# Kernel optimization log

Hardware: AMD Instinct MI355X
Metric: run time of the kernel (lower is better)

Reference implementation:

```python
import jax, jax.numpy as jnp
import numpy as np

B, S, H = 2, 2048, 1024
E, I, K = 8, 4096, 2


def setup_inputs() -> dict:
    key = jax.random.key(0)
    ks = jax.random.split(key, 5)
    scale_h = 1.0 / np.sqrt(H)
    scale_i = 1.0 / np.sqrt(I)
    x = jax.random.normal(ks[0], (B, S, H), dtype=jnp.float32)
    gate_w = jax.random.normal(ks[1], (E, H), dtype=jnp.float32) * scale_h   # router Linear weight [out=E, in=H]
    wg = jax.random.normal(ks[2], (E, I, H), dtype=jnp.float32) * scale_h    # gate_proj weights, stacked over experts
    wu = jax.random.normal(ks[3], (E, I, H), dtype=jnp.float32) * scale_h    # up_proj weights
    wd = jax.random.normal(ks[4], (E, H, I), dtype=jnp.float32) * scale_i    # down_proj weights
    return {"x": x, "gate_w": gate_w, "wg": wg, "wu": wu, "wd": wd}


def _moe_forward(x, gate_w, wg, wu, wd):
    b, s, h = x.shape
    x_flat = x.reshape(-1, h)                       # [T, H]
    logits = x_flat @ gate_w.T                      # [T, E]
    top_v, top_i = jax.lax.top_k(logits, K)         # [T, K]
    probs = jax.nn.softmax(top_v.astype(jnp.float32), axis=-1).astype(logits.dtype)  # [T, K]
    # per-token combine weight for each expert: sum_k probs[:,k] * 1[top_i[:,k]==e]
    one_hot = jax.nn.one_hot(top_i, E, dtype=probs.dtype)   # [T, K, E]
    combine = jnp.einsum('tk,tke->et', probs, one_hot)       # [E, T]
    # loop over experts via scan: acc += w_e * SwiGLU_e(x)
    def body(acc, ws):
        wge, wue, wde, we = ws
        hidden = jax.nn.silu(x_flat @ wge.T) * (x_flat @ wue.T)  # [T, I]
        return acc + we[:, None] * (hidden @ wde.T), None
    out, _ = jax.lax.scan(body, jnp.zeros_like(x_flat), (wg, wu, wd, combine))
    return out.reshape(b, s, h)


def reference(x, gate_w, wg, wu, wd):
    return _moe_forward(x, gate_w, wg, wu, wd)
```

## Files before the change

kernel.cpp:

```cpp
#include <hip/hip_runtime.h>
#include <math.h>

#define T_TOK 4096
#define H_DIM 1024
#define E_NUM 8
#define I_DIM 4096

typedef __attribute__((ext_vector_type(4))) float f32x4;
typedef __attribute__((ext_vector_type(8))) short bf16x8;

__device__ inline unsigned short f2bf(float f) {
  unsigned int u = __float_as_uint(f);
  u += 0x7fffu + ((u >> 16) & 1u);
  return (unsigned short)(u >> 16);
}

__device__ inline void cvt_store4(unsigned short* dst, const float* src) {
  f32x4 v = *reinterpret_cast<const f32x4*>(src);
  ushort4 o;
  o.x = f2bf(v[0]); o.y = f2bf(v[1]); o.z = f2bf(v[2]); o.w = f2bf(v[3]);
  *reinterpret_cast<ushort4*>(dst) = o;
}

__device__ inline void gll16(const void* g, void* l) {
  __builtin_amdgcn_global_load_lds(
      (const __attribute__((address_space(1))) void*)g,
      (__attribute__((address_space(3))) void*)l, 16, 0, 0);
}

__global__ __launch_bounds__(64) void k_router(const float* __restrict__ x,
                                               const float* __restrict__ gw,
                                               int2* __restrict__ tokE,
                                               float2* __restrict__ tokP,
                                               int* __restrict__ counts) {
  const int t = blockIdx.x;
  const int l = threadIdx.x;
  const float* xr = x + (size_t)t * H_DIM;
  float acc[E_NUM];
#pragma unroll
  for (int e = 0; e < E_NUM; e++) acc[e] = 0.f;
  for (int h = l; h < H_DIM; h += 64) {
    float xv = xr[h];
#pragma unroll
    for (int e = 0; e < E_NUM; e++) acc[e] += xv * gw[e * H_DIM + h];
  }
#pragma unroll
  for (int e = 0; e < E_NUM; e++) {
#pragma unroll
    for (int off = 32; off > 0; off >>= 1) acc[e] += __shfl_xor(acc[e], off);
  }
  if (l == 0) {
    float v0 = -1e30f, v1 = -1e30f;
    int e0 = 0, e1 = 0;
#pragma unroll
    for (int e = 0; e < E_NUM; e++) {
      float v = acc[e];
      if (v > v0) { v1 = v0; e1 = e0; v0 = v; e0 = e; }
      else if (v > v1) { v1 = v; e1 = e; }
    }
    float ex = expf(v1 - v0);
    float p0 = 1.f / (1.f + ex);
    float p1 = ex * p0;
    tokE[t] = make_int2(e0, e1);
    tokP[t] = make_float2(p0, p1);
    atomicAdd(&counts[e0], 1);
    atomicAdd(&counts[e1], 1);
  }
}

__global__ void k_offsets(const int* __restrict__ counts, int* __restrict__ offsets) {
  if (threadIdx.x == 0 && blockIdx.x == 0) {
    int s = 0;
    for (int e = 0; e < E_NUM; e++) { offsets[e] = s; s += counts[e]; }
    offsets[E_NUM] = s;
  }
}

__global__ __launch_bounds__(256) void k_scatter(const int2* __restrict__ tokE,
                                                 const float2* __restrict__ tokP,
                                                 const int* __restrict__ offsets,
                                                 int* __restrict__ cursor,
                                                 int* __restrict__ slot_tok,
                                                 float* __restrict__ slot_w) {
  int t = blockIdx.x * 256 + threadIdx.x;
  if (t >= T_TOK) return;
  int2 e = tokE[t];
  float2 p = tokP[t];
  int pos0 = atomicAdd(&cursor[e.x], 1);
  slot_tok[offsets[e.x] + pos0] = t;
  slot_w[offsets[e.x] + pos0] = p.x;
  int pos1 = atomicAdd(&cursor[e.y], 1);
  slot_tok[offsets[e.y] + pos1] = t;
  slot_w[offsets[e.y] + pos1] = p.y;
}

__global__ __launch_bounds__(256) void k_cvt(const float* __restrict__ src,
                                             unsigned short* __restrict__ dst,
                                             int n4) {
  int i = blockIdx.x * 256 + threadIdx.x;
  const int stride = gridDim.x * 256;
  for (; i < n4; i += stride) {
    f32x4 v = reinterpret_cast<const f32x4*>(src)[i];
    ushort4 o;
    o.x = f2bf(v[0]); o.y = f2bf(v[1]); o.z = f2bf(v[2]); o.w = f2bf(v[3]);
    reinterpret_cast<ushort4*>(dst)[i] = o;
  }
}

__global__ __launch_bounds__(256, 2) void k_gateup2(
    const unsigned short* __restrict__ xb, const unsigned short* __restrict__ wgb,
    const unsigned short* __restrict__ wub, const int* __restrict__ counts,
    const int* __restrict__ offsets, const int* __restrict__ slot_tok,
    unsigned short* __restrict__ hidden) {
  const int e = blockIdx.z;
  const int cnt = counts[e];
  const int m0 = blockIdx.y * 128;
  if (m0 >= cnt) return;
  const int n0 = blockIdx.x * 128;
  const int base = offsets[e];

  __shared__ unsigned short As[128 * 64];
  __shared__ unsigned short Bg[128 * 64];
  __shared__ unsigned short Bu[128 * 64];

  const int tid = threadIdx.x;
  const int wave = tid >> 6;
  const int lane = tid & 63;
  const int wm = (wave >> 1) * 64;
  const int wn = (wave & 1) * 64;
  const int lr = lane & 15;
  const int lk = lane >> 4;

  const int sr = lane >> 3;
  const int sc = lane & 7;
  const int swz = ((sc ^ sr) << 3);

  const size_t wbase = (size_t)e * I_DIM * H_DIM;
  const unsigned short* srcA[4];
  const unsigned short* srcBg[4];
  const unsigned short* srcBu[4];
  unsigned short* dstA[4];
  unsigned short* dstBg[4];
  unsigned short* dstBu[4];
#pragma unroll
  for (int i = 0; i < 4; i++) {
    int row = wave * 32 + i * 8 + sr;
    int gr = m0 + row; if (gr > cnt - 1) gr = cnt - 1;
    srcA[i]  = xb + (size_t)slot_tok[base + gr] * H_DIM + swz;
    srcBg[i] = wgb + wbase + (size_t)(n0 + row) * H_DIM + swz;
    srcBu[i] = wub + wbase + (size_t)(n0 + row) * H_DIM + swz;
    dstA[i]  = &As[(wave * 32 + i * 8) * 64];
    dstBg[i] = &Bg[(wave * 32 + i * 8) * 64];
    dstBu[i] = &Bu[(wave * 32 + i * 8) * 64];
  }

  f32x4 accg[4][4], accu[4][4];
#pragma unroll
  for (int i = 0; i < 4; i++)
#pragma unroll
    for (int j = 0; j < 4; j++) {
      accg[i][j] = (f32x4){0.f, 0.f, 0.f, 0.f};
      accu[i][j] = (f32x4){0.f, 0.f, 0.f, 0.f};
    }

  const int xorr = ((lr & 7) << 3);

  for (int k0 = 0; k0 < H_DIM; k0 += 64) {
#pragma unroll
    for (int i = 0; i < 4; i++) {
      gll16(srcA[i] + k0, dstA[i]);
      gll16(srcBg[i] + k0, dstBg[i]);
      gll16(srcBu[i] + k0, dstBu[i]);
    }
    __syncthreads();
#pragma unroll
    for (int kh = 0; kh < 2; kh++) {
      const int koff = (((kh * 4 + lk) << 3) ^ xorr);
      bf16x8 af[4];
#pragma unroll
      for (int mf = 0; mf < 4; mf++)
        af[mf] = *reinterpret_cast<const bf16x8*>(&As[(wm + mf * 16 + lr) * 64 + koff]);
#pragma unroll
      for (int nf = 0; nf < 4; nf++) {
        const int roff = (wn + nf * 16 + lr) * 64 + koff;
        bf16x8 bg = *reinterpret_cast<const bf16x8*>(&Bg[roff]);
        bf16x8 bu = *reinterpret_cast<const bf16x8*>(&Bu[roff]);
#pragma unroll
        for (int mf = 0; mf < 4; mf++) {
          accg[mf][nf] = __builtin_amdgcn_mfma_f32_16x16x32_bf16(af[mf], bg, accg[mf][nf], 0, 0, 0);
          accu[mf][nf] = __builtin_amdgcn_mfma_f32_16x16x32_bf16(af[mf], bu, accu[mf][nf], 0, 0, 0);
        }
      }
    }
    __syncthreads();
  }

#pragma unroll
  for (int mf = 0; mf < 4; mf++) {
#pragma unroll
    for (int j = 0; j < 4; j++) {
      int row = wm + mf * 16 + lk * 4 + j;
      if (m0 + row < cnt) {
        size_t hbase = (size_t)(base + m0 + row) * I_DIM;
#pragma unroll
        for (int nf = 0; nf < 4; nf++) {
          int col = n0 + wn + nf * 16 + lr;
          float g = accg[mf][nf][j];
          float u = accu[mf][nf][j];
          float h = g / (1.f + expf(-g)) * u;
          hidden[hbase + col] = f2bf(h);
        }
      }
    }
  }
}

__global__ __launch_bounds__(256, 2) void k_down2(
    const unsigned short* __restrict__ hidden, const unsigned short* __restrict__ wdb,
    const int* __restrict__ counts, const int* __restrict__ offsets,
    const int* __restrict__ slot_tok, const float* __restrict__ slot_w,
    float* __restrict__ out) {
  const int e = blockIdx.z;
  const int cnt = counts[e];
  const int m0 = blockIdx.y * 128;
  if (m0 >= cnt) return;
  const int n0 = blockIdx.x * 128;
  const int base = offsets[e];

  __shared__ unsigned short As[128 * 64];
  __shared__ unsigned short Bs[128 * 64];

  const int tid = threadIdx.x;
  const int wave = tid >> 6;
  const int lane = tid & 63;
  const int wm = (wave >> 1) * 64;
  const int wn = (wave & 1) * 64;
  const int lr = lane & 15;
  const int lk = lane >> 4;

  const int sr = lane >> 3;
  const int sc = lane & 7;
  const int swz = ((sc ^ sr) << 3);

  const unsigned short* srcA[4];
  const unsigned short* srcB[4];
  unsigned short* dstA[4];
  unsigned short* dstB[4];
#pragma unroll
  for (int i = 0; i < 4; i++) {
    int row = wave * 32 + i * 8 + sr;
    int gr = m0 + row; if (gr > cnt - 1) gr = cnt - 1;
    srcA[i] = hidden + (size_t)(base + gr) * I_DIM + swz;
    srcB[i] = wdb + (size_t)e * H_DIM * I_DIM + (size_t)(n0 + row) * I_DIM + swz;
    dstA[i] = &As[(wave * 32 + i * 8) * 64];
    dstB[i] = &Bs[(wave * 32 + i * 8) * 64];
  }

  f32x4 acc[4][4];
#pragma unroll
  for (int i = 0; i < 4; i++)
#pragma unroll
    for (int j = 0; j < 4; j++) acc[i][j] = (f32x4){0.f, 0.f, 0.f, 0.f};

  const int xorr = ((lr & 7) << 3);

  for (int k0 = 0; k0 < I_DIM; k0 += 64) {
#pragma unroll
    for (int i = 0; i < 4; i++) {
      gll16(srcA[i] + k0, dstA[i]);
      gll16(srcB[i] + k0, dstB[i]);
    }
    __syncthreads();
#pragma unroll
    for (int kh = 0; kh < 2; kh++) {
      const int koff = (((kh * 4 + lk) << 3) ^ xorr);
      bf16x8 af[4];
#pragma unroll
      for (int mf = 0; mf < 4; mf++)
        af[mf] = *reinterpret_cast<const bf16x8*>(&As[(wm + mf * 16 + lr) * 64 + koff]);
#pragma unroll
      for (int nf = 0; nf < 4; nf++) {
        bf16x8 bf = *reinterpret_cast<const bf16x8*>(&Bs[(wn + nf * 16 + lr) * 64 + koff]);
#pragma unroll
        for (int mf = 0; mf < 4; mf++)
          acc[mf][nf] = __builtin_amdgcn_mfma_f32_16x16x32_bf16(af[mf], bf, acc[mf][nf], 0, 0, 0);
      }
    }
    __syncthreads();
  }

#pragma unroll
  for (int mf = 0; mf < 4; mf++) {
#pragma unroll
    for (int j = 0; j < 4; j++) {
      int row = wm + mf * 16 + lk * 4 + j;
      if (m0 + row < cnt) {
        int slot = base + m0 + row;
        int t = slot_tok[slot];
        float w = slot_w[slot];
#pragma unroll
        for (int nf = 0; nf < 4; nf++) {
          int col = n0 + wn + nf * 16 + lr;
          atomicAdd(&out[(size_t)t * H_DIM + col], w * acc[mf][nf][j]);
        }
      }
    }
  }
}

__global__ __launch_bounds__(256) void k_gateup_v1(
    const float* __restrict__ x, const float* __restrict__ wg,
    const float* __restrict__ wu, const int* __restrict__ counts,
    const int* __restrict__ offsets, const int* __restrict__ slot_tok,
    unsigned short* __restrict__ hidden) {
  const int e = blockIdx.z;
  const int cnt = counts[e];
  const int m0 = blockIdx.y * 128;
  if (m0 >= cnt) return;
  const int n0 = blockIdx.x * 128;
  const int base = offsets[e];

  __shared__ unsigned short As[128 * 40];
  __shared__ unsigned short Bgs[128 * 40];
  __shared__ unsigned short Bus[128 * 40];

  const int tid = threadIdx.x;
  const int wave = tid >> 6;
  const int lane = tid & 63;
  const int wm = (wave >> 1) * 64;
  const int wn = (wave & 1) * 64;
  const int lr = lane & 15;
  const int lk = lane >> 4;
  const int r_sub = tid >> 3;
  const int kq = (tid & 7) * 4;

  const float* wge = wg + (size_t)e * I_DIM * H_DIM;
  const float* wue = wu + (size_t)e * I_DIM * H_DIM;

  const float* aptr[4];
  const float* bgptr[4];
  const float* buptr[4];
#pragma unroll
  for (int p = 0; p < 4; p++) {
    int row = p * 32 + r_sub;
    int gr = m0 + row;
    if (gr > cnt - 1) gr = cnt - 1;
    aptr[p] = x + (size_t)slot_tok[base + gr] * H_DIM + kq;
    bgptr[p] = wge + (size_t)(n0 + row) * H_DIM + kq;
    buptr[p] = wue + (size_t)(n0 + row) * H_DIM + kq;
  }

  f32x4 accg[4][4], accu[4][4];
#pragma unroll
  for (int i = 0; i < 4; i++)
#pragma unroll
    for (int j = 0; j < 4; j++) {
      accg[i][j] = (f32x4){0.f, 0.f, 0.f, 0.f};
      accu[i][j] = (f32x4){0.f, 0.f, 0.f, 0.f};
    }

  for (int k0 = 0; k0 < H_DIM; k0 += 32) {
#pragma unroll
    for (int p = 0; p < 4; p++) {
      int row = p * 32 + r_sub;
      cvt_store4(&As[row * 40 + kq], aptr[p] + k0);
      cvt_store4(&Bgs[row * 40 + kq], bgptr[p] + k0);
      cvt_store4(&Bus[row * 40 + kq], buptr[p] + k0);
    }
    __syncthreads();
    bf16x8 af[4];
#pragma unroll
    for (int mf = 0; mf < 4; mf++)
      af[mf] = *reinterpret_cast<const bf16x8*>(&As[(wm + mf * 16 + lr) * 40 + lk * 8]);
#pragma unroll
    for (int nf = 0; nf < 4; nf++) {
      bf16x8 bg = *reinterpret_cast<const bf16x8*>(&Bgs[(wn + nf * 16 + lr) * 40 + lk * 8]);
      bf16x8 bu = *reinterpret_cast<const bf16x8*>(&Bus[(wn + nf * 16 + lr) * 40 + lk * 8]);
#pragma unroll
      for (int mf = 0; mf < 4; mf++) {
        accg[mf][nf] = __builtin_amdgcn_mfma_f32_16x16x32_bf16(af[mf], bg, accg[mf][nf], 0, 0, 0);
        accu[mf][nf] = __builtin_amdgcn_mfma_f32_16x16x32_bf16(af[mf], bu, accu[mf][nf], 0, 0, 0);
      }
    }
    __syncthreads();
  }

#pragma unroll
  for (int mf = 0; mf < 4; mf++) {
#pragma unroll
    for (int j = 0; j < 4; j++) {
      int row = wm + mf * 16 + lk * 4 + j;
      if (m0 + row < cnt) {
        size_t hbase = (size_t)(base + m0 + row) * I_DIM;
#pragma unroll
        for (int nf = 0; nf < 4; nf++) {
          int col = n0 + wn + nf * 16 + lr;
          float g = accg[mf][nf][j];
          float u = accu[mf][nf][j];
          float h = g / (1.f + expf(-g)) * u;
          hidden[hbase + col] = f2bf(h);
        }
      }
    }
  }
}

__global__ __launch_bounds__(256) void k_down_v1(
    const unsigned short* __restrict__ hidden, const float* __restrict__ wd,
    const int* __restrict__ counts, const int* __restrict__ offsets,
    const int* __restrict__ slot_tok, const float* __restrict__ slot_w,
    float* __restrict__ out) {
  const int e = blockIdx.z;
  const int cnt = counts[e];
  const int m0 = blockIdx.y * 128;
  if (m0 >= cnt) return;
  const int n0 = blockIdx.x * 128;
  const int base = offsets[e];

  __shared__ unsigned short As[128 * 40];
  __shared__ unsigned short Bs[128 * 40];

  const int tid = threadIdx.x;
  const int wave = tid >> 6;
  const int lane = tid & 63;
  const int wm = (wave >> 1) * 64;
  const int wn = (wave & 1) * 64;
  const int lr = lane & 15;
  const int lk = lane >> 4;
  const int r_sub = tid >> 3;
  const int kq = (tid & 7) * 4;

  const unsigned short* ap[4];
  const float* bp[4];
#pragma unroll
  for (int p = 0; p < 4; p++) {
    int row = p * 32 + r_sub;
    int gr = m0 + row;
    if (gr > cnt - 1) gr = cnt - 1;
    ap[p] = hidden + (size_t)(base + gr) * I_DIM + kq;
    bp[p] = wd + (size_t)e * H_DIM * I_DIM + (size_t)(n0 + row) * I_DIM + kq;
  }

  f32x4 acc[4][4];
#pragma unroll
  for (int i = 0; i < 4; i++)
#pragma unroll
    for (int j = 0; j < 4; j++) acc[i][j] = (f32x4){0.f, 0.f, 0.f, 0.f};

  for (int k0 = 0; k0 < I_DIM; k0 += 32) {
#pragma unroll
    for (int p = 0; p < 4; p++) {
      int row = p * 32 + r_sub;
      *reinterpret_cast<ushort4*>(&As[row * 40 + kq]) =
          *reinterpret_cast<const ushort4*>(ap[p] + k0);
      cvt_store4(&Bs[row * 40 + kq], bp[p] + k0);
    }
    __syncthreads();
    bf16x8 af[4];
#pragma unroll
    for (int mf = 0; mf < 4; mf++)
      af[mf] = *reinterpret_cast<const bf16x8*>(&As[(wm + mf * 16 + lr) * 40 + lk * 8]);
#pragma unroll
    for (int nf = 0; nf < 4; nf++) {
      bf16x8 bf = *reinterpret_cast<const bf16x8*>(&Bs[(wn + nf * 16 + lr) * 40 + lk * 8]);
#pragma unroll
      for (int mf = 0; mf < 4; mf++)
        acc[mf][nf] = __builtin_amdgcn_mfma_f32_16x16x32_bf16(af[mf], bf, acc[mf][nf], 0, 0, 0);
    }
    __syncthreads();
  }

#pragma unroll
  for (int mf = 0; mf < 4; mf++) {
#pragma unroll
    for (int j = 0; j < 4; j++) {
      int row = wm + mf * 16 + lk * 4 + j;
      if (m0 + row < cnt) {
        int slot = base + m0 + row;
        int t = slot_tok[slot];
        float w = slot_w[slot];
#pragma unroll
        for (int nf = 0; nf < 4; nf++) {
          int col = n0 + wn + nf * 16 + lr;
          atomicAdd(&out[(size_t)t * H_DIM + col], w * acc[mf][nf][j]);
        }
      }
    }
  }
}

extern "C" void kernel_launch(void* const* d_in, const int* in_sizes, int n_in,
                              void* d_out, int out_size, void* d_ws, size_t ws_size,
                              hipStream_t stream) {
  const float* x = (const float*)d_in[0];
  const float* gate_w = (const float*)d_in[1];
  const float* wg = (const float*)d_in[2];
  const float* wu = (const float*)d_in[3];
  const float* wd = (const float*)d_in[4];
  float* out = (float*)d_out;

  char* ws = (char*)d_ws;
  int* counts = (int*)(ws + 0);
  int* cursor = (int*)(ws + 64);
  int* offsets = (int*)(ws + 128);
  int2* tokE = (int2*)(ws + 256);
  float2* tokP = (float2*)(ws + 256 + 32768);
  int* slot_tok = (int*)(ws + 256 + 65536);
  float* slot_w = (float*)(ws + 256 + 98304);

  hipMemsetAsync(d_ws, 0, 256, stream);
  hipMemsetAsync(d_out, 0, (size_t)T_TOK * H_DIM * sizeof(float), stream);

  k_router<<<T_TOK, 64, 0, stream>>>(x, gate_w, tokE, tokP, counts);
  k_offsets<<<1, 64, 0, stream>>>(counts, offsets);
  k_scatter<<<T_TOK / 256, 256, 0, stream>>>(tokE, tokP, offsets, cursor, slot_tok, slot_w);

  const size_t OFF_XB  = 262144;
  const size_t OFF_HID = OFF_XB + 8388608;
  const size_t OFF_WG  = OFF_HID + 67108864;
  const size_t OFF_WU  = OFF_WG + 67108864;
  const size_t NEED    = OFF_WU + 67108864;

  if (ws_size >= NEED) {
    unsigned short* xb  = (unsigned short*)(ws + OFF_XB);
    unsigned short* hid = (unsigned short*)(ws + OFF_HID);
    unsigned short* wgb = (unsigned short*)(ws + OFF_WG);
    unsigned short* wub = (unsigned short*)(ws + OFF_WU);
    unsigned short* wdb = wgb;

    k_cvt<<<2048, 256, 0, stream>>>(x, xb, T_TOK * H_DIM / 4);
    k_cvt<<<2048, 256, 0, stream>>>(wg, wgb, E_NUM * I_DIM * H_DIM / 4);
    k_cvt<<<2048, 256, 0, stream>>>(wu, wub, E_NUM * I_DIM * H_DIM / 4);
    k_gateup2<<<dim3(I_DIM / 128, 32, E_NUM), 256, 0, stream>>>(
        xb, wgb, wub, counts, offsets, slot_tok, hid);
    k_cvt<<<2048, 256, 0, stream>>>(wd, wdb, E_NUM * H_DIM * I_DIM / 4);
    k_down2<<<dim3(H_DIM / 128, 32, E_NUM), 256, 0, stream>>>(
        hid, wdb, counts, offsets, slot_tok, slot_w, out);
  } else {
    unsigned short* hid = (unsigned short*)(ws + 131328);
    k_gateup_v1<<<dim3(I_DIM / 128, 32, E_NUM), 256, 0, stream>>>(
        x, wg, wu, counts, offsets, slot_tok, hid);
    k_down_v1<<<dim3(H_DIM / 128, 32, E_NUM), 256, 0, stream>>>(
        hid, wd, counts, offsets, slot_tok, slot_w, out);
  }
}
```

Measured before the change: 563.5 us.

## Rewrite MoE GEMMs as 8-wave double-buffered 256x128 tiles with phased prefetch

```diff
diff --git a/kernel.cpp b/kernel.cpp
--- a/kernel.cpp
+++ b/kernel.cpp
@@ -107,190 +107,279 @@
   }
 }
 
-__global__ __launch_bounds__(256, 2) void k_gateup2(
+
+__global__ __launch_bounds__(512, 2) void k_gateup8(
     const unsigned short* __restrict__ xb, const unsigned short* __restrict__ wgb,
     const unsigned short* __restrict__ wub, const int* __restrict__ counts,
     const int* __restrict__ offsets, const int* __restrict__ slot_tok,
     unsigned short* __restrict__ hidden) {
   const int e = blockIdx.z;
   const int cnt = counts[e];
-  const int m0 = blockIdx.y * 128;
+  const int m0 = blockIdx.y * 256;
   if (m0 >= cnt) return;
   const int n0 = blockIdx.x * 128;
   const int base = offsets[e];
 
-  __shared__ unsigned short As[128 * 64];
-  __shared__ unsigned short Bg[128 * 64];
-  __shared__ unsigned short Bu[128 * 64];
+  __shared__ unsigned short As[2][256 * 64];
+  __shared__ unsigned short Bgs[2][128 * 64];
+  __shared__ unsigned short Bus[2][128 * 64];
 
   const int tid = threadIdx.x;
   const int wave = tid >> 6;
   const int lane = tid & 63;
-  const int wm = (wave >> 1) * 64;
-  const int wn = (wave & 1) * 64;
+  const int wm = (wave >> 2) * 128;
+  const int wn = (wave & 3) * 32;
   const int lr = lane & 15;
   const int lk = lane >> 4;
-
-  const int sr = lane >> 3;
-  const int sc = lane & 7;
-  const int swz = ((sc ^ sr) << 3);
-
-  const size_t wbase = (size_t)e * I_DIM * H_DIM;
-  const unsigned short* srcA[4];
-  const unsigned short* srcBg[4];
-  const unsigned short* srcBu[4];
-  unsigned short* dstA[4];
-  unsigned short* dstBg[4];
-  unsigned short* dstBu[4];
+  const int xr = lr & 7;
+
+  const int srow = lane >> 3;
+  const int schk = lane & 7;
+  const int swz = ((schk ^ srow) << 3);
+  const int ldsw = wave * 8 * 64;
+
+  const size_t wboff = (size_t)e * (size_t)I_DIM * H_DIM;
+  const unsigned short* pA[4];
+  const unsigned short* pBg[2];
+  const unsigned short* pBu[2];
 #pragma unroll
   for (int i = 0; i < 4; i++) {
-    int row = wave * 32 + i * 8 + sr;
-    int gr = m0 + row; if (gr > cnt - 1) gr = cnt - 1;
-    srcA[i]  = xb + (size_t)slot_tok[base + gr] * H_DIM + swz;
-    srcBg[i] = wgb + wbase + (size_t)(n0 + row) * H_DIM + swz;
-    srcBu[i] = wub + wbase + (size_t)(n0 + row) * H_DIM + swz;
-    dstA[i]  = &As[(wave * 32 + i * 8) * 64];
-    dstBg[i] = &Bg[(wave * 32 + i * 8) * 64];
-    dstBu[i] = &Bu[(wave * 32 + i * 8) * 64];
-  }
-
-  f32x4 accg[4][4], accu[4][4];
-#pragma unroll
-  for (int i = 0; i < 4; i++)
-#pragma unroll
-    for (int j = 0; j < 4; j++) {
+    int r = i * 64 + wave * 8 + srow;
+    int gr = m0 + r; if (gr > cnt - 1) gr = cnt - 1;
+    pA[i] = xb + (size_t)slot_tok[base + gr] * H_DIM + swz;
+  }
+#pragma unroll
+  for (int i = 0; i < 2; i++) {
+    int r = i * 64 + wave * 8 + srow;
+    pBg[i] = wgb + wboff + (size_t)(n0 + r) * H_DIM + swz;
+    pBu[i] = wub + wboff + (size_t)(n0 + r) * H_DIM + swz;
+  }
+
+  f32x4 accg[8][2], accu[8][2];
+#pragma unroll
+  for (int i = 0; i < 8; i++)
+#pragma unroll
+    for (int j = 0; j < 2; j++) {
       accg[i][j] = (f32x4){0.f, 0.f, 0.f, 0.f};
       accu[i][j] = (f32x4){0.f, 0.f, 0.f, 0.f};
     }
 
-  const int xorr = ((lr & 7) << 3);
-
-  for (int k0 = 0; k0 < H_DIM; k0 += 64) {
-#pragma unroll
-    for (int i = 0; i < 4; i++) {
-      gll16(srcA[i] + k0, dstA[i]);
-      gll16(srcBg[i] + k0, dstBg[i]);
-      gll16(srcBu[i] + k0, dstBu[i]);
-    }
-    __syncthreads();
-#pragma unroll
-    for (int kh = 0; kh < 2; kh++) {
-      const int koff = (((kh * 4 + lk) << 3) ^ xorr);
-      bf16x8 af[4];
-#pragma unroll
-      for (int mf = 0; mf < 4; mf++)
-        af[mf] = *reinterpret_cast<const bf16x8*>(&As[(wm + mf * 16 + lr) * 64 + koff]);
-#pragma unroll
-      for (int nf = 0; nf < 4; nf++) {
-        const int roff = (wn + nf * 16 + lr) * 64 + koff;
-        bf16x8 bg = *reinterpret_cast<const bf16x8*>(&Bg[roff]);
-        bf16x8 bu = *reinterpret_cast<const bf16x8*>(&Bu[roff]);
-#pragma unroll
-        for (int mf = 0; mf < 4; mf++) {
-          accg[mf][nf] = __builtin_amdgcn_mfma_f32_16x16x32_bf16(af[mf], bg, accg[mf][nf], 0, 0, 0);
-          accu[mf][nf] = __builtin_amdgcn_mfma_f32_16x16x32_bf16(af[mf], bu, accu[mf][nf], 0, 0, 0);
-        }
-      }
-    }
-    __syncthreads();
-  }
-
-#pragma unroll
-  for (int mf = 0; mf < 4; mf++) {
+  const int ar = (wm + lr) * 64;
+  const int br = (wn + lr) * 64;
+  const int c0 = ((lk ^ xr) << 3);
+  const int c1 = (((4 + lk) ^ xr) << 3);
+
+  bf16x8 fg[2][2], fu[2][2];
+
+  gll16(pBg[0], &Bgs[0][0 * 4096 + ldsw]);
+  gll16(pBg[1], &Bgs[0][1 * 4096 + ldsw]);
+  gll16(pBu[0], &Bus[0][0 * 4096 + ldsw]);
+  gll16(pBu[1], &Bus[0][1 * 4096 + ldsw]);
+  gll16(pA[0], &As[0][0 * 4096 + ldsw]);
+  gll16(pA[2], &As[0][2 * 4096 + ldsw]);
+  gll16(pA[1], &As[0][1 * 4096 + ldsw]);
+  gll16(pA[3], &As[0][3 * 4096 + ldsw]);
+
+#define GU_PHASE(P, CUR, NXT, KNXT)                                            \
+  do {                                                                         \
+    if ((P) == 0) {                                                            \
+      gll16(pBg[0] + (KNXT), &Bgs[NXT][0 * 4096 + ldsw]);                      \
+      gll16(pBg[1] + (KNXT), &Bgs[NXT][1 * 4096 + ldsw]);                      \
+      asm volatile("s_waitcnt vmcnt(4)" ::: "memory");                         \
+    } else if ((P) == 1) {                                                     \
+      gll16(pBu[0] + (KNXT), &Bus[NXT][0 * 4096 + ldsw]);                      \
+      gll16(pBu[1] + (KNXT), &Bus[NXT][1 * 4096 + ldsw]);                      \
+    } else if ((P) == 2) {                                                     \
+      gll16(pA[0] + (KNXT), &As[NXT][0 * 4096 + ldsw]);                        \
+      gll16(pA[2] + (KNXT), &As[NXT][2 * 4096 + ldsw]);                        \
+      asm volatile("s_waitcnt vmcnt(6)" ::: "memory");                         \
+    } else {                                                                   \
+      gll16(pA[1] + (KNXT), &As[NXT][1 * 4096 + ldsw]);                        \
+      gll16(pA[3] + (KNXT), &As[NXT][3 * 4096 + ldsw]);                        \
+    }                                                                          \
+    __builtin_amdgcn_s_barrier();                                              \
+    if ((P) == 0) {                                                            \
+      _Pragma("unroll") for (int nf = 0; nf < 2; nf++) {                       \
+        fg[nf][0] = *(const bf16x8*)&Bgs[CUR][br + nf * 1024 + c0];            \
+        fg[nf][1] = *(const bf16x8*)&Bgs[CUR][br + nf * 1024 + c1];            \
+        fu[nf][0] = *(const bf16x8*)&Bus[CUR][br + nf * 1024 + c0];            \
+        fu[nf][1] = *(const bf16x8*)&Bus[CUR][br + nf * 1024 + c1];            \
+      }                                                                        \
+    }                                                                          \
+    bf16x8 a00 = *(const bf16x8*)&As[CUR][ar + (2 * (P)) * 1024 + c0];         \
+    bf16x8 a01 = *(const bf16x8*)&As[CUR][ar + (2 * (P)) * 1024 + c1];         \
+    bf16x8 a10 = *(const bf16x8*)&As[CUR][ar + (2 * (P) + 1) * 1024 + c0];     \
+    bf16x8 a11 = *(const bf16x8*)&As[CUR][ar + (2 * (P) + 1) * 1024 + c1];     \
+    __builtin_amdgcn_s_setprio(1);                                             \
+    _Pragma("unroll") for (int nf = 0; nf < 2; nf++) {                         \
+      accg[2*(P)][nf]   = __builtin_amdgcn_mfma_f32_16x16x32_bf16(a00, fg[nf][0], accg[2*(P)][nf], 0, 0, 0);     \
+      accg[2*(P)][nf]   = __builtin_amdgcn_mfma_f32_16x16x32_bf16(a01, fg[nf][1], accg[2*(P)][nf], 0, 0, 0);     \
+      accu[2*(P)][nf]   = __builtin_amdgcn_mfma_f32_16x16x32_bf16(a00, fu[nf][0], accu[2*(P)][nf], 0, 0, 0);     \
+      accu[2*(P)][nf]   = __builtin_amdgcn_mfma_f32_16x16x32_bf16(a01, fu[nf][1], accu[2*(P)][nf], 0, 0, 0);     \
+      accg[2*(P)+1][nf] = __builtin_amdgcn_mfma_f32_16x16x32_bf16(a10, fg[nf][0], accg[2*(P)+1][nf], 0, 0, 0);   \
+      accg[2*(P)+1][nf] = __builtin_amdgcn_mfma_f32_16x16x32_bf16(a11, fg[nf][1], accg[2*(P)+1][nf], 0, 0, 0);   \
+      accu[2*(P)+1][nf] = __builtin_amdgcn_mfma_f32_16x16x32_bf16(a10, fu[nf][0], accu[2*(P)+1][nf], 0, 0, 0);   \
+      accu[2*(P)+1][nf] = __builtin_amdgcn_mfma_f32_16x16x32_bf16(a11, fu[nf][1], accu[2*(P)+1][nf], 0, 0, 0);   \
+    }                                                                          \
+    __builtin_amdgcn_s_setprio(0);                                             \
+    __builtin_amdgcn_s_barrier();                                              \
+  } while (0)
+
+#define GU_STEP(CUR, NXT, KNXT) \
+  GU_PHASE(0, CUR, NXT, KNXT);  \
+  GU_PHASE(1, CUR, NXT, KNXT);  \
+  GU_PHASE(2, CUR, NXT, KNXT);  \
+  GU_PHASE(3, CUR, NXT, KNXT);
+
+  for (int t = 0; t < 16; t += 2) {
+    const int k1 = (t + 1) * 64;
+    const int k2 = (t + 2 < 16) ? (t + 2) * 64 : 0;
+    GU_STEP(0, 1, k1);
+    GU_STEP(1, 0, k2);
+  }
+#undef GU_PHASE
+#undef GU_STEP
+
+#pragma unroll
+  for (int mf = 0; mf < 8; mf++) {
 #pragma unroll
     for (int j = 0; j < 4; j++) {
       int row = wm + mf * 16 + lk * 4 + j;
       if (m0 + row < cnt) {
         size_t hbase = (size_t)(base + m0 + row) * I_DIM;
 #pragma unroll
-        for (int nf = 0; nf < 4; nf++) {
+        for (int nf = 0; nf < 2; nf++) {
           int col = n0 + wn + nf * 16 + lr;
           float g = accg[mf][nf][j];
           float u = accu[mf][nf][j];
-          float h = g / (1.f + expf(-g)) * u;
-          hidden[hbase + col] = f2bf(h);
+          hidden[hbase + col] = f2bf(g / (1.f + expf(-g)) * u);
         }
       }
     }
   }
 }
 
-__global__ __launch_bounds__(256, 2) void k_down2(
+__global__ __launch_bounds__(512, 2) void k_down8(
     const unsigned short* __restrict__ hidden, const unsigned short* __restrict__ wdb,
     const int* __restrict__ counts, const int* __restrict__ offsets,
     const int* __restrict__ slot_tok, const float* __restrict__ slot_w,
     float* __restrict__ out) {
   const int e = blockIdx.z;
   const int cnt = counts[e];
-  const int m0 = blockIdx.y * 128;
+  const int m0 = blockIdx.y * 256;
   if (m0 >= cnt) return;
   const int n0 = blockIdx.x * 128;
   const int base = offsets[e];
 
-  __shared__ unsigned short As[128 * 64];
-  __shared__ unsigned short Bs[128 * 64];
+  __shared__ unsigned short As[2][256 * 64];
+  __shared__ unsigned short Bs[2][128 * 64];
 
   const int tid = threadIdx.x;
   const int wave = tid >> 6;
   const int lane = tid & 63;
-  const int wm = (wave >> 1) * 64;
-  const int wn = (wave & 1) * 64;
+  const int wm = (wave >> 2) * 128;
+  const int wn = (wave & 3) * 32;
   const int lr = lane & 15;
   const int lk = lane >> 4;
-
-  const int sr = lane >> 3;
-  const int sc = lane & 7;
-  const int swz = ((sc ^ sr) << 3);
-
-  const unsigned short* srcA[4];
-  const unsigned short* srcB[4];
-  unsigned short* dstA[4];
-  unsigned short* dstB[4];
+  const int xr = lr & 7;
+
+  const int srow = lane >> 3;
+  const int schk = lane & 7;
+  const int swz = ((schk ^ srow) << 3);
+  const int ldsw = wave * 8 * 64;
+
+  const unsigned short* pA[4];
+  const unsigned short* pB[2];
 #pragma unroll
   for (int i = 0; i < 4; i++) {
-    int row = wave * 32 + i * 8 + sr;
-    int gr = m0 + row; if (gr > cnt - 1) gr = cnt - 1;
-    srcA[i] = hidden + (size_t)(base + gr) * I_DIM + swz;
-    srcB[i] = wdb + (size_t)e * H_DIM * I_DIM + (size_t)(n0 + row) * I_DIM + swz;
-    dstA[i] = &As[(wave * 32 + i * 8) * 64];
-    dstB[i] = &Bs[(wave * 32 + i * 8) * 64];
-  }
-
-  f32x4 acc[4][4];
-#pragma unroll
-  for (int i = 0; i < 4; i++)
-#pragma unroll
-    for (int j = 0; j < 4; j++) acc[i][j] = (f32x4){0.f, 0.f, 0.f, 0.f};
-
-  const int xorr = ((lr & 7) << 3);
-
-  for (int k0 = 0; k0 < I_DIM; k0 += 64) {
-#pragma unroll
-    for (int i = 0; i < 4; i++) {
-      gll16(srcA[i] + k0, dstA[i]);
-      gll16(srcB[i] + k0, dstB[i]);
-    }
-    __syncthreads();
-#pragma unroll
-    for (int kh = 0; kh < 2; kh++) {
-      const int koff = (((kh * 4 + lk) << 3) ^ xorr);
-      bf16x8 af[4];
-#pragma unroll
-      for (int mf = 0; mf < 4; mf++)
-        af[mf] = *reinterpret_cast<const bf16x8*>(&As[(wm + mf * 16 + lr) * 64 + koff]);
-#pragma unroll
-      for (int nf = 0; nf < 4; nf++) {
-        bf16x8 bf = *reinterpret_cast<const bf16x8*>(&Bs[(wn + nf * 16 + lr) * 64 + koff]);
-#pragma unroll
-        for (int mf = 0; mf < 4; mf++)
-          acc[mf][nf] = __builtin_amdgcn_mfma_f32_16x16x32_bf16(af[mf], bf, acc[mf][nf], 0, 0, 0);
-      }
-    }
-    __syncthreads();
-  }
-
-#pragma unroll
-  for (int mf = 0; mf < 4; mf++) {
+    int r = i * 64 + wave * 8 + srow;
+    int gr = m0 + r; if (gr > cnt - 1) gr = cnt - 1;
+    pA[i] = hidden + (size_t)(base + gr) * I_DIM + swz;
+  }
+#pragma unroll
+  for (int i = 0; i < 2; i++) {
+    int r = i * 64 + wave * 8 + srow;
+    pB[i] = wdb + (size_t)e * H_DIM * I_DIM + (size_t)(n0 + r) * I_DIM + swz;
+  }
+
+  f32x4 acc[8][2];
+#pragma unroll
+  for (int i = 0; i < 8; i++)
+#pragma unroll
+    for (int j = 0; j < 2; j++) acc[i][j] = (f32x4){0.f, 0.f, 0.f, 0.f};
+
+  const int ar = (wm + lr) * 64;
+  const int br = (wn + lr) * 64;
+  const int c0 = ((lk ^ xr) << 3);
+  const int c1 = (((4 + lk) ^ xr) << 3);
+
+  bf16x8 fb[2][2];
+
+  gll16(pB[0], &Bs[0][0 * 4096 + ldsw]);
+  gll16(pB[1], &Bs[0][1 * 4096 + ldsw]);
+  gll16(pA[0], &As[0][0 * 4096 + ldsw]);
+  gll16(pA[2], &As[0][2 * 4096 + ldsw]);
+  gll16(pA[1], &As[0][1 * 4096 + ldsw]);
+  gll16(pA[3], &As[0][3 * 4096 + ldsw]);
+
+#define DN_PHASE(P, CUR, NXT, KNXT)                                            \
+  do {                                                                         \
+    if ((P) == 0) {                                                            \
+      gll16(pB[0] + (KNXT), &Bs[NXT][0 * 4096 + ldsw]);                        \
+      gll16(pB[1] + (KNXT), &Bs[NXT][1 * 4096 + ldsw]);                        \
+      gll16(pA[0] + (KNXT), &As[NXT][0 * 4096 + ldsw]);                        \
+      asm volatile("s_waitcnt vmcnt(5)" ::: "memory");                         \
+    } else {                                                                   \
+      gll16(pA[2] + (KNXT), &As[NXT][2 * 4096 + ldsw]);                        \
+      gll16(pA[1] + (KNXT), &As[NXT][1 * 4096 + ldsw]);                        \
+      gll16(pA[3] + (KNXT), &As[NXT][3 * 4096 + ldsw]);                        \
+      asm volatile("s_waitcnt vmcnt(6)" ::: "memory");                         \
+    }                                                                          \
+    __builtin_amdgcn_s_barrier();                                              \
+    if ((P) == 0) {                                                            \
+      _Pragma("unroll") for (int nf = 0; nf < 2; nf++) {                       \
+        fb[nf][0] = *(const bf16x8*)&Bs[CUR][br + nf * 1024 + c0];             \
+        fb[nf][1] = *(const bf16x8*)&Bs[CUR][br + nf * 1024 + c1];             \
+      }                                                                        \
+    }                                                                          \
+    bf16x8 a0k0 = *(const bf16x8*)&As[CUR][ar + (4 * (P) + 0) * 1024 + c0];    \
+    bf16x8 a0k1 = *(const bf16x8*)&As[CUR][ar + (4 * (P) + 0) * 1024 + c1];    \
+    bf16x8 a1k0 = *(const bf16x8*)&As[CUR][ar + (4 * (P) + 1) * 1024 + c0];    \
+    bf16x8 a1k1 = *(const bf16x8*)&As[CUR][ar + (4 * (P) + 1) * 1024 + c1];    \
+    bf16x8 a2k0 = *(const bf16x8*)&As[CUR][ar + (4 * (P) + 2) * 1024 + c0];    \
+    bf16x8 a2k1 = *(const bf16x8*)&As[CUR][ar + (4 * (P) + 2) * 1024 + c1];    \
+    bf16x8 a3k0 = *(const bf16x8*)&As[CUR][ar + (4 * (P) + 3) * 1024 + c0];    \
+    bf16x8 a3k1 = *(const bf16x8*)&As[CUR][ar + (4 * (P) + 3) * 1024 + c1];    \
+    __builtin_amdgcn_s_setprio(1);                                             \
+    _Pragma("unroll") for (int nf = 0; nf < 2; nf++) {                         \
+      acc[4*(P)+0][nf] = __builtin_amdgcn_mfma_f32_16x16x32_bf16(a0k0, fb[nf][0], acc[4*(P)+0][nf], 0, 0, 0);  \
+      acc[4*(P)+0][nf] = __builtin_amdgcn_mfma_f32_16x16x32_bf16(a0k1, fb[nf][1], acc[4*(P)+0][nf], 0, 0, 0);  \
+      acc[4*(P)+1][nf] = __builtin_amdgcn_mfma_f32_16x16x32_bf16(a1k0, fb[nf][0], acc[4*(P)+1][nf], 0, 0, 0);  \
+      acc[4*(P)+1][nf] = __builtin_amdgcn_mfma_f32_16x16x32_bf16(a1k1, fb[nf][1], acc[4*(P)+1][nf], 0, 0, 0);  \
+      acc[4*(P)+2][nf] = __builtin_amdgcn_mfma_f32_16x16x32_bf16(a2k0, fb[nf][0], acc[4*(P)+2][nf], 0, 0, 0);  \
+      acc[4*(P)+2][nf] = __builtin_amdgcn_mfma_f32_16x16x32_bf16(a2k1, fb[nf][1], acc[4*(P)+2][nf], 0, 0, 0);  \
+      acc[4*(P)+3][nf] = __builtin_amdgcn_mfma_f32_16x16x32_bf16(a3k0, fb[nf][0], acc[4*(P)+3][nf], 0, 0, 0);  \
+      acc[4*(P)+3][nf] = __builtin_amdgcn_mfma_f32_16x16x32_bf16(a3k1, fb[nf][1], acc[4*(P)+3][nf], 0, 0, 0);  \
+    }                                                                          \
+    __builtin_amdgcn_s_setprio(0);                                             \
+    __builtin_amdgcn_s_barrier();                                              \
+  } while (0)
+
+#define DN_STEP(CUR, NXT, KNXT) \
+  DN_PHASE(0, CUR, NXT, KNXT);  \
+  DN_PHASE(1, CUR, NXT, KNXT);
+
+  for (int t = 0; t < 64; t += 2) {
+    const int k1 = (t + 1) * 64;
+    const int k2 = (t + 2 < 64) ? (t + 2) * 64 : 0;
+    DN_STEP(0, 1, k1);
+    DN_STEP(1, 0, k2);
+  }
+#undef DN_PHASE
+#undef DN_STEP
+
+#pragma unroll
+  for (int mf = 0; mf < 8; mf++) {
 #pragma unroll
     for (int j = 0; j < 4; j++) {
       int row = wm + mf * 16 + lk * 4 + j;
@@ -299,7 +388,7 @@
         int t = slot_tok[slot];
         float w = slot_w[slot];
 #pragma unroll
-        for (int nf = 0; nf < 4; nf++) {
+        for (int nf = 0; nf < 2; nf++) {
           int col = n0 + wn + nf * 16 + lr;
           atomicAdd(&out[(size_t)t * H_DIM + col], w * acc[mf][nf][j]);
         }
@@ -531,10 +620,10 @@
     k_cvt<<<2048, 256, 0, stream>>>(x, xb, T_TOK * H_DIM / 4);
     k_cvt<<<2048, 256, 0, stream>>>(wg, wgb, E_NUM * I_DIM * H_DIM / 4);
     k_cvt<<<2048, 256, 0, stream>>>(wu, wub, E_NUM * I_DIM * H_DIM / 4);
-    k_gateup2<<<dim3(I_DIM / 128, 32, E_NUM), 256, 0, stream>>>(
+    k_gateup8<<<dim3(I_DIM / 128, 16, E_NUM), 512, 0, stream>>>(
         xb, wgb, wub, counts, offsets, slot_tok, hid);
     k_cvt<<<2048, 256, 0, stream>>>(wd, wdb, E_NUM * H_DIM * I_DIM / 4);
-    k_down2<<<dim3(H_DIM / 128, 32, E_NUM), 256, 0, stream>>>(
+    k_down8<<<dim3(H_DIM / 128, 16, E_NUM), 512, 0, stream>>>(
         hid, wdb, counts, offsets, slot_tok, slot_w, out);
   } else {
     unsigned short* hid = (unsigned short*)(ws + 131328);
```

Result: slower. 695.3 us (+23.4%).

## Double-buffer LDS tiles with async prefetch in gate-up and down GEMMs

Applied to the files above, without the earlier changes.

```diff
diff --git a/kernel.cpp b/kernel.cpp
--- a/kernel.cpp
+++ b/kernel.cpp
@@ -107,7 +107,8 @@
   }
 }
 
-__global__ __launch_bounds__(256, 2) void k_gateup2(
+
+__global__ __launch_bounds__(256, 2) void k_gateup3(
     const unsigned short* __restrict__ xb, const unsigned short* __restrict__ wgb,
     const unsigned short* __restrict__ wub, const int* __restrict__ counts,
     const int* __restrict__ offsets, const int* __restrict__ slot_tok,
@@ -119,9 +120,9 @@
   const int n0 = blockIdx.x * 128;
   const int base = offsets[e];
 
-  __shared__ unsigned short As[128 * 64];
-  __shared__ unsigned short Bg[128 * 64];
-  __shared__ unsigned short Bu[128 * 64];
+  __shared__ unsigned short As[2][128 * 32];
+  __shared__ unsigned short Bg[2][128 * 32];
+  __shared__ unsigned short Bu[2][128 * 32];
 
   const int tid = threadIdx.x;
   const int wave = tid >> 6;
@@ -131,27 +132,22 @@
   const int lr = lane & 15;
   const int lk = lane >> 4;
 
-  const int sr = lane >> 3;
-  const int sc = lane & 7;
-  const int swz = ((sc ^ sr) << 3);
-
-  const size_t wbase = (size_t)e * I_DIM * H_DIM;
-  const unsigned short* srcA[4];
-  const unsigned short* srcBg[4];
-  const unsigned short* srcBu[4];
-  unsigned short* dstA[4];
-  unsigned short* dstBg[4];
-  unsigned short* dstBu[4];
-#pragma unroll
-  for (int i = 0; i < 4; i++) {
-    int row = wave * 32 + i * 8 + sr;
+  const int sr = lane >> 2;
+  const int sc = lane & 3;
+  const int swz = ((sc ^ (sr & 3)) << 3);
+
+  const size_t wboff = (size_t)e * (size_t)I_DIM * H_DIM;
+  const unsigned short* srcA[2];
+  const unsigned short* srcBg[2];
+  const unsigned short* srcBu[2];
+  const int dstoff[2] = {(wave * 32) * 32, (wave * 32 + 16) * 32};
+#pragma unroll
+  for (int i = 0; i < 2; i++) {
+    int row = wave * 32 + i * 16 + sr;
     int gr = m0 + row; if (gr > cnt - 1) gr = cnt - 1;
     srcA[i]  = xb + (size_t)slot_tok[base + gr] * H_DIM + swz;
-    srcBg[i] = wgb + wbase + (size_t)(n0 + row) * H_DIM + swz;
-    srcBu[i] = wub + wbase + (size_t)(n0 + row) * H_DIM + swz;
-    dstA[i]  = &As[(wave * 32 + i * 8) * 64];
-    dstBg[i] = &Bg[(wave * 32 + i * 8) * 64];
-    dstBu[i] = &Bu[(wave * 32 + i * 8) * 64];
+    srcBg[i] = wgb + wboff + (size_t)(n0 + row) * H_DIM + swz;
+    srcBu[i] = wub + wboff + (size_t)(n0 + row) * H_DIM + swz;
   }
 
   f32x4 accg[4][4], accu[4][4];
@@ -163,37 +159,51 @@
       accu[i][j] = (f32x4){0.f, 0.f, 0.f, 0.f};
     }
 
-  const int xorr = ((lr & 7) << 3);
-
-  for (int k0 = 0; k0 < H_DIM; k0 += 64) {
-#pragma unroll
-    for (int i = 0; i < 4; i++) {
-      gll16(srcA[i] + k0, dstA[i]);
-      gll16(srcBg[i] + k0, dstBg[i]);
-      gll16(srcBu[i] + k0, dstBu[i]);
-    }
-    __syncthreads();
-#pragma unroll
-    for (int kh = 0; kh < 2; kh++) {
-      const int koff = (((kh * 4 + lk) << 3) ^ xorr);
-      bf16x8 af[4];
-#pragma unroll
-      for (int mf = 0; mf < 4; mf++)
-        af[mf] = *reinterpret_cast<const bf16x8*>(&As[(wm + mf * 16 + lr) * 64 + koff]);
-#pragma unroll
-      for (int nf = 0; nf < 4; nf++) {
-        const int roff = (wn + nf * 16 + lr) * 64 + koff;
-        bf16x8 bg = *reinterpret_cast<const bf16x8*>(&Bg[roff]);
-        bf16x8 bu = *reinterpret_cast<const bf16x8*>(&Bu[roff]);
-#pragma unroll
-        for (int mf = 0; mf < 4; mf++) {
-          accg[mf][nf] = __builtin_amdgcn_mfma_f32_16x16x32_bf16(af[mf], bg, accg[mf][nf], 0, 0, 0);
-          accu[mf][nf] = __builtin_amdgcn_mfma_f32_16x16x32_bf16(af[mf], bu, accu[mf][nf], 0, 0, 0);
-        }
+  const int koff = ((lk ^ (lr & 3)) << 3);
+
+  asm volatile("s_waitcnt vmcnt(0)" ::: "memory");
+
+  gll16(srcBg[0], &Bg[0][dstoff[0]]);
+  gll16(srcBg[1], &Bg[0][dstoff[1]]);
+  gll16(srcBu[0], &Bu[0][dstoff[0]]);
+  gll16(srcBu[1], &Bu[0][dstoff[1]]);
+  gll16(srcA[0],  &As[0][dstoff[0]]);
+  gll16(srcA[1],  &As[0][dstoff[1]]);
+
+  const int NT = H_DIM / 32;
+  for (int t = 0; t < NT; t++) {
+    const int bb = t & 1;
+    const int nb = bb ^ 1;
+    const int kn = (t + 1 < NT) ? (t + 1) * 32 : 0;
+    gll16(srcBg[0] + kn, &Bg[nb][dstoff[0]]);
+    gll16(srcBg[1] + kn, &Bg[nb][dstoff[1]]);
+    gll16(srcBu[0] + kn, &Bu[nb][dstoff[0]]);
+    gll16(srcBu[1] + kn, &Bu[nb][dstoff[1]]);
+    gll16(srcA[0] + kn,  &As[nb][dstoff[0]]);
+    gll16(srcA[1] + kn,  &As[nb][dstoff[1]]);
+    asm volatile("s_waitcnt vmcnt(6)" ::: "memory");
+    __builtin_amdgcn_s_barrier();
+
+    bf16x8 af[4];
+#pragma unroll
+    for (int mf = 0; mf < 4; mf++)
+      af[mf] = *reinterpret_cast<const bf16x8*>(&As[bb][(wm + mf * 16 + lr) * 32 + koff]);
+    __builtin_amdgcn_s_setprio(1);
+#pragma unroll
+    for (int nf = 0; nf < 4; nf++) {
+      const int ro = (wn + nf * 16 + lr) * 32 + koff;
+      bf16x8 bg = *reinterpret_cast<const bf16x8*>(&Bg[bb][ro]);
+      bf16x8 bu = *reinterpret_cast<const bf16x8*>(&Bu[bb][ro]);
+#pragma unroll
+      for (int mf = 0; mf < 4; mf++) {
+        accg[mf][nf] = __builtin_amdgcn_mfma_f32_16x16x32_bf16(af[mf], bg, accg[mf][nf], 0, 0, 0);
+        accu[mf][nf] = __builtin_amdgcn_mfma_f32_16x16x32_bf16(af[mf], bu, accu[mf][nf], 0, 0, 0);
       }
     }
-    __syncthreads();
-  }
+    __builtin_amdgcn_s_setprio(0);
+    __builtin_amdgcn_s_barrier();
+  }
+  asm volatile("s_waitcnt vmcnt(0)" ::: "memory");
 
 #pragma unroll
   for (int mf = 0; mf < 4; mf++) {
@@ -207,15 +217,14 @@
           int col = n0 + wn + nf * 16 + lr;
           float g = accg[mf][nf][j];
           float u = accu[mf][nf][j];
-          float h = g / (1.f + expf(-g)) * u;
-          hidden[hbase + col] = f2bf(h);
+          hidden[hbase + col] = f2bf(g / (1.f + expf(-g)) * u);
         }
       }
     }
   }
 }
 
-__global__ __launch_bounds__(256, 2) void k_down2(
+__global__ __launch_bounds__(256, 2) void k_down3(
     const unsigned short* __restrict__ hidden, const unsigned short* __restrict__ wdb,
     const int* __restrict__ counts, const int* __restrict__ offsets,
     const int* __restrict__ slot_tok, const float* __restrict__ slot_w,
@@ -227,8 +236,8 @@
   const int n0 = blockIdx.x * 128;
   const int base = offsets[e];
 
-  __shared__ unsigned short As[128 * 64];
-  __shared__ unsigned short Bs[128 * 64];
+  __shared__ unsigned short As[2][128 * 32];
+  __shared__ unsigned short Bs[2][128 * 32];
 
   const int tid = threadIdx.x;
   const int wave = tid >> 6;
@@ -238,22 +247,19 @@
   const int lr = lane & 15;
   const int lk = lane >> 4;
 
-  const int sr = lane >> 3;
-  const int sc = lane & 7;
-  const int swz = ((sc ^ sr) << 3);
-
-  const unsigned short* srcA[4];
-  const unsigned short* srcB[4];
-  unsigned short* dstA[4];
-  unsigned short* dstB[4];
-#pragma unroll
-  for (int i = 0; i < 4; i++) {
-    int row = wave * 32 + i * 8 + sr;
+  const int sr = lane >> 2;
+  const int sc = lane & 3;
+  const int swz = ((sc ^ (sr & 3)) << 3);
+
+  const unsigned short* srcA[2];
+  const unsigned short* srcB[2];
+  const int dstoff[2] = {(wave * 32) * 32, (wave * 32 + 16) * 32};
+#pragma unroll
+  for (int i = 0; i < 2; i++) {
+    int row = wave * 32 + i * 16 + sr;
     int gr = m0 + row; if (gr > cnt - 1) gr = cnt - 1;
     srcA[i] = hidden + (size_t)(base + gr) * I_DIM + swz;
     srcB[i] = wdb + (size_t)e * H_DIM * I_DIM + (size_t)(n0 + row) * I_DIM + swz;
-    dstA[i] = &As[(wave * 32 + i * 8) * 64];
-    dstB[i] = &Bs[(wave * 32 + i * 8) * 64];
   }
 
   f32x4 acc[4][4];
@@ -262,32 +268,43 @@
 #pragma unroll
     for (int j = 0; j < 4; j++) acc[i][j] = (f32x4){0.f, 0.f, 0.f, 0.f};
 
-  const int xorr = ((lr & 7) << 3);
-
-  for (int k0 = 0; k0 < I_DIM; k0 += 64) {
-#pragma unroll
-    for (int i = 0; i < 4; i++) {
-      gll16(srcA[i] + k0, dstA[i]);
-      gll16(srcB[i] + k0, dstB[i]);
-    }
-    __syncthreads();
-#pragma unroll
-    for (int kh = 0; kh < 2; kh++) {
-      const int koff = (((kh * 4 + lk) << 3) ^ xorr);
-      bf16x8 af[4];
+  const int koff = ((lk ^ (lr & 3)) << 3);
+
+  asm volatile("s_waitcnt vmcnt(0)" ::: "memory");
+
+  gll16(srcB[0], &Bs[0][dstoff[0]]);
+  gll16(srcB[1], &Bs[0][dstoff[1]]);
+  gll16(srcA[0], &As[0][dstoff[0]]);
+  gll16(srcA[1], &As[0][dstoff[1]]);
+
+  const int NT = I_DIM / 32;
+  for (int t = 0; t < NT; t++) {
+    const int bb = t & 1;
+    const int nb = bb ^ 1;
+    const int kn = (t + 1 < NT) ? (t + 1) * 32 : 0;
+    gll16(srcB[0] + kn, &Bs[nb][dstoff[0]]);
+    gll16(srcB[1] + kn, &Bs[nb][dstoff[1]]);
+    gll16(srcA[0] + kn, &As[nb][dstoff[0]]);
+    gll16(srcA[1] + kn, &As[nb][dstoff[1]]);
+    asm volatile("s_waitcnt vmcnt(4)" ::: "memory");
+    __builtin_amdgcn_s_barrier();
+
+    bf16x8 af[4];
+#pragma unroll
+    for (int mf = 0; mf < 4; mf++)
+      af[mf] = *reinterpret_cast<const bf16x8*>(&As[bb][(wm + mf * 16 + lr) * 32 + koff]);
+    __builtin_amdgcn_s_setprio(1);
+#pragma unroll
+    for (int nf = 0; nf < 4; nf++) {
+      bf16x8 bf = *reinterpret_cast<const bf16x8*>(&Bs[bb][(wn + nf * 16 + lr) * 32 + koff]);
 #pragma unroll
       for (int mf = 0; mf < 4; mf++)
-        af[mf] = *reinterpret_cast<const bf16x8*>(&As[(wm + mf * 16 + lr) * 64 + koff]);
-#pragma unroll
-      for (int nf = 0; nf < 4; nf++) {
-        bf16x8 bf = *reinterpret_cast<const bf16x8*>(&Bs[(wn + nf * 16 + lr) * 64 + koff]);
-#pragma unroll
-        for (int mf = 0; mf < 4; mf++)
-          acc[mf][nf] = __builtin_amdgcn_mfma_f32_16x16x32_bf16(af[mf], bf, acc[mf][nf], 0, 0, 0);
-      }
-    }
-    __syncthreads();
-  }
+        acc[mf][nf] = __builtin_amdgcn_mfma_f32_16x16x32_bf16(af[mf], bf, acc[mf][nf], 0, 0, 0);
+    }
+    __builtin_amdgcn_s_setprio(0);
+    __builtin_amdgcn_s_barrier();
+  }
+  asm volatile("s_waitcnt vmcnt(0)" ::: "memory");
 
 #pragma unroll
   for (int mf = 0; mf < 4; mf++) {
@@ -531,10 +548,10 @@
     k_cvt<<<2048, 256, 0, stream>>>(x, xb, T_TOK * H_DIM / 4);
     k_cvt<<<2048, 256, 0, stream>>>(wg, wgb, E_NUM * I_DIM * H_DIM / 4);
     k_cvt<<<2048, 256, 0, stream>>>(wu, wub, E_NUM * I_DIM * H_DIM / 4);
-    k_gateup2<<<dim3(I_DIM / 128, 32, E_NUM), 256, 0, stream>>>(
+    k_gateup3<<<dim3(I_DIM / 128, 32, E_NUM), 256, 0, stream>>>(
         xb, wgb, wub, counts, offsets, slot_tok, hid);
     k_cvt<<<2048, 256, 0, stream>>>(wd, wdb, E_NUM * H_DIM * I_DIM / 4);
-    k_down2<<<dim3(H_DIM / 128, 32, E_NUM), 256, 0, stream>>>(
+    k_down3<<<dim3(H_DIM / 128, 32, E_NUM), 256, 0, stream>>>(
         hid, wdb, counts, offsets, slot_tok, slot_w, out);
   } else {
     unsigned short* hid = (unsigned short*)(ws + 131328);
```

Measured after the change: 642.3 us. 14.0% more time.
